# Kernel tuning notes

Measured on AMD Instinct MI355X. Metric: run time of the kernel, lower is better.

The kernel has to match this reference:

```python
import jax, jax.numpy as jnp
import numpy as np

B, L, E, V, H, M, O = 16, 64, 256, 16000, 8, 4, 2
DH = E // H
START = 0

def _pe():
    pos = np.arange(L, dtype=np.float32)[:, None]
    div = np.exp(np.arange(0, E, 2, dtype=np.float32) * (-np.log(10000.0) / E))
    pe = np.zeros((L, E), dtype=np.float32)
    pe[:, 0::2] = np.sin(pos * div)
    pe[:, 1::2] = np.cos(pos * div)
    return jnp.asarray(pe)

PE = _pe()  # [L, E] sinusoidal positional encoding (dropout p=0.0)


def setup_inputs() -> dict:
    key = jax.random.key(0)
    ks = jax.random.split(key, 16)
    g = lambda k, sh, sc: jax.random.normal(k, sh, jnp.float32) * sc
    return {
        'noise': jax.random.normal(ks[0], (B, L), jnp.float32),
        'inEmb_W': g(ks[1], (M, L, L), 1.0 / np.sqrt(L)),   # M stacked Linear(L, L), [in,out] layout
        'inEmb_b': jnp.zeros((M, L), jnp.float32),
        'Wq': g(ks[2], (O, E, E), 1.0 / np.sqrt(E)),
        'bq': jnp.zeros((O, E), jnp.float32),
        'Wk': g(ks[3], (O, E, E), 1.0 / np.sqrt(E)),
        'bk': jnp.zeros((O, E), jnp.float32),
        'Wv': g(ks[4], (O, E, E), 1.0 / np.sqrt(E)),
        'bv': jnp.zeros((O, E), jnp.float32),
        'Wo': g(ks[5], (O, E, E), 1.0 / np.sqrt(E)),
        'bo': jnp.zeros((O, E), jnp.float32),
        'ln_g': jnp.ones((O, E), jnp.float32),
        'ln_b': jnp.zeros((O, E), jnp.float32),
        'emb': g(ks[6], (V, E), 1.0),                       # Word2Vec embedding table
        'soft_W': g(ks[7], (E, V), 1.0 / np.sqrt(E)),       # soft head Linear(E, V)
        'soft_b': jnp.zeros((V,), jnp.float32),
    }


def _ln(x, g, b):
    mu = x.mean(-1, keepdims=True)
    var = ((x - mu) ** 2).mean(-1, keepdims=True)
    return (x - mu) / jnp.sqrt(var + 1e-5) * g + b


def _mha_norm(kv, q, Wq, bq, Wk, bk, Wv, bv, Wo, bo, g, b, kmask):
    # MHAwithNorm: attn(query=q, key=kv, value=kv) -> out proj -> residual -> LayerNorm
    Q = (q @ Wq + bq).reshape(B, L, H, DH)
    K = (kv @ Wk + bk).reshape(B, L, H, DH)
    Vh = (kv @ Wv + bv).reshape(B, L, H, DH)
    s = jnp.einsum('bqhd,bkhd->bhqk', Q, K) / np.sqrt(DH)
    s = jnp.where(kmask[None, None, None, :], s, -1e9)  # only the tok generated positions are valid keys
    a = jax.nn.softmax(s, axis=-1)
    o = jnp.einsum('bhqk,bkhd->bqhd', a, Vh).reshape(B, L, E)
    return _ln(o @ Wo + bo + q, g, b)


def _decode(noise, inEmb_W, inEmb_b, Wq, bq, Wk, bk, Wv, bv, Wo, bo, ln_g, ln_b, emb, soft_W, soft_b):
    w = noise
    for i in range(M):
        w = w @ inEmb_W[i] + inEmb_b[i]
    w = jnp.broadcast_to(w[:, :, None], (B, L, E))  # unsqueeze(-1).repeat(1,1,E)

    Y0 = jnp.zeros((B, L, E), jnp.float32).at[:, 0].set(emb[START] + PE[0])

    def step(Y, tok):
        kmask = jnp.arange(L) < tok  # current sequence length == tok
        out = Y
        for i in range(O):  # cross-attn blocks against w[:, :tok]
            out = _mha_norm(w, out, Wq[i], bq[i], Wk[i], bk[i], Wv[i], bv[i], Wo[i], bo[i], ln_g[i], ln_b[i], kmask)
        for i in range(O):  # same blocks reused as self-attn (faithful to source)
            out = _mha_norm(out, out, Wq[i], bq[i], Wk[i], bk[i], Wv[i], bv[i], Wo[i], bo[i], ln_g[i], ln_b[i], kmask)
        logits = out[:, tok - 1] @ soft_W + soft_b
        probs = jax.nn.softmax(logits, axis=-1)
        nxt = jnp.argmax(probs, axis=-1)  # [B]
        Y = Y.at[:, tok].set(emb[nxt] + PE[tok])
        return Y, (nxt, probs)

    _, (toks, probs) = jax.lax.scan(step, Y0, jnp.arange(1, L))
    return toks, probs  # toks [L-1, B] int, probs [L-1, B, V]


def reference(noise, inEmb_W, inEmb_b, Wq, bq, Wk, bk, Wv, bv, Wo, bo, ln_g, ln_b, emb, soft_W, soft_b):
    toks, _ = _decode(noise, inEmb_W, inEmb_b, Wq, bq, Wk, bk, Wv, bv, Wo, bo, ln_g, ln_b, emb, soft_W, soft_b)
    # torch.stack(out_sent[0]): generated token ids of batch element 0, incl. <START>
    return jnp.concatenate([jnp.array([START], dtype=toks.dtype), toks[:, 0]])
```

## Files before the change

### kernel.cpp

```cpp
#include <hip/hip_runtime.h>
#include <stdint.h>


#define NWG 128
#define NT 256

__device__ __forceinline__ float ld_c(const float* p){
  return __hip_atomic_load(p, __ATOMIC_RELAXED, __HIP_MEMORY_SCOPE_AGENT);
}
__device__ __forceinline__ void st_c(float* p, float v){
  __hip_atomic_store(p, v, __ATOMIC_RELAXED, __HIP_MEMORY_SCOPE_AGENT);
}
__device__ __forceinline__ int ld_fi(const int* p){
  return __hip_atomic_load(p, __ATOMIC_RELAXED, __HIP_MEMORY_SCOPE_AGENT);
}
__device__ __forceinline__ void st_fi(int* p, int v){
  __hip_atomic_store(p, v, __ATOMIC_RELAXED, __HIP_MEMORY_SCOPE_AGENT);
}

__device__ __forceinline__ float wredsum(float v){
#pragma unroll
  for (int m=32;m;m>>=1) v += __shfl_xor(v,m,64);
  return v;
}
__device__ __forceinline__ float wredmax(float v){
#pragma unroll
  for (int m=32;m;m>>=1) v = fmaxf(v,__shfl_xor(v,m,64));
  return v;
}
__device__ __forceinline__ float g32sum(float v){
#pragma unroll
  for (int m=16;m;m>>=1) v += __shfl_xor(v,m,64);
  return v;
}
__device__ __forceinline__ float g32max(float v){
#pragma unroll
  for (int m=16;m;m>>=1) v = fmaxf(v,__shfl_xor(v,m,64));
  return v;
}
__device__ __forceinline__ unsigned long long shflx64(unsigned long long v,int m){
  unsigned int lo=(unsigned int)(v&0xffffffffull), hi=(unsigned int)(v>>32);
  lo=__shfl_xor(lo,m,64); hi=__shfl_xor(hi,m,64);
  return (((unsigned long long)hi)<<32)|(unsigned long long)lo;
}

__device__ __forceinline__ float pe_val(int l, int e){
  int j = e >> 1;
  float dv = expf((float)(2*j) * (-0.035977892078031970f));
  float arg = (float)l * dv;
  return (e & 1) ? cosf(arg) : sinf(arg);
}

__device__ __forceinline__ void gbar_f(int* arr, int* rel, int ep){
  __syncthreads();
  if (threadIdx.x==0){
    __builtin_amdgcn_fence(__ATOMIC_RELEASE, "agent");
    __hip_atomic_store(arr + blockIdx.x*16, ep, __ATOMIC_RELAXED, __HIP_MEMORY_SCOPE_AGENT);
  }
  if (blockIdx.x==0){
    if (threadIdx.x < NWG){
      while (__hip_atomic_load(arr + threadIdx.x*16, __ATOMIC_RELAXED, __HIP_MEMORY_SCOPE_AGENT) != ep)
        __builtin_amdgcn_s_sleep(1);
    }
    __syncthreads();
    if (threadIdx.x==0)
      __hip_atomic_store(rel, ep, __ATOMIC_RELAXED, __HIP_MEMORY_SCOPE_AGENT);
  }
  if (threadIdx.x==0){
    while (__hip_atomic_load(rel, __ATOMIC_RELAXED, __HIP_MEMORY_SCOPE_AGENT) != ep)
      __builtin_amdgcn_s_sleep(1);
    __builtin_amdgcn_fence(__ATOMIC_ACQUIRE, "agent");
  }
  __syncthreads();
}

__device__ __forceinline__ void gbar_nf(int* arr, int* rel, int ep){
  __syncthreads();
  if (threadIdx.x==0)
    __hip_atomic_store(arr + blockIdx.x*16, ep, __ATOMIC_RELAXED, __HIP_MEMORY_SCOPE_AGENT);
  if (blockIdx.x==0){
    if (threadIdx.x < NWG){
      while (__hip_atomic_load(arr + threadIdx.x*16, __ATOMIC_RELAXED, __HIP_MEMORY_SCOPE_AGENT) != ep)
        __builtin_amdgcn_s_sleep(1);
    }
    __syncthreads();
    if (threadIdx.x==0)
      __hip_atomic_store(rel, ep, __ATOMIC_RELAXED, __HIP_MEMORY_SCOPE_AGENT);
  }
  if (threadIdx.x==0){
    while (__hip_atomic_load(rel, __ATOMIC_RELAXED, __HIP_MEMORY_SCOPE_AGENT) != ep)
      __builtin_amdgcn_s_sleep(1);
  }
  __syncthreads();
}

extern "C" __global__ __launch_bounds__(256, 2)
void gen18124_kernel(const float* __restrict__ noise,
                     const float* __restrict__ iw, const float* __restrict__ ib,
                     const float* __restrict__ Wq, const float* __restrict__ bq,
                     const float* __restrict__ Wk, const float* __restrict__ bk,
                     const float* __restrict__ Wv, const float* __restrict__ bv,
                     const float* __restrict__ Wo, const float* __restrict__ bo,
                     const float* __restrict__ lng, const float* __restrict__ lnb,
                     const float* __restrict__ emb, const float* __restrict__ sw,
                     const float* __restrict__ sb,
                     int* __restrict__ out, float* __restrict__ ws)
{
  const float ISQ = 0.17677669529663687f;
  __shared__ float sm[5376];
  __shared__ unsigned long long redU[4];
  extern __shared__ float swl[];

  float* WVEC = ws;
  float* SKC  = ws+64;
  float* SVC  = ws+576;
  float* KAP  = ws+1088;
  float* UT   = ws+5184;
  float* CC   = ws+9280;
  float* BETA = ws+9792;
  unsigned long long* SLOTS = (unsigned long long*)(ws+9824);
  int* Z3F = (int*)(ws+9952);
  int* ARR = (int*)(ws+10080);
  int* REL = (int*)(ws+12128);
  float* Yg  = ws+14208;
  float* R1  = ws+30592;
  float* QB  = ws+46976;
  float* KB  = ws+63360;
  float* VB  = ws+79744;
  float* R2  = ws+96128;
  float* Z2P = ws+112512;
  float* Z3P = ws+243584;

  const int g = blockIdx.x, t = threadIdx.x;
  int ep = 0;

  {
    const int base = g*125;
#pragma unroll 8
    for (int i=t; i<256*128; i+=NT){
      int e=i>>7, c=i&127;
      float val = 0.f;
      if (c<125) val = sw[e*16000 + base + c];
      swl[i]=val;
    }
  }

  {
    int c0 = 2*g;
    float a0=Wk[t*256+c0],       a1=Wk[t*256+c0+1];
    float a2=Wk[65536+t*256+c0], a3=Wk[65536+t*256+c0+1];
    float a4=Wv[t*256+c0],       a5=Wv[t*256+c0+1];
    float a6=Wv[65536+t*256+c0], a7=Wv[65536+t*256+c0+1];
    a0=wredsum(a0); a1=wredsum(a1); a2=wredsum(a2); a3=wredsum(a3);
    a4=wredsum(a4); a5=wredsum(a5); a6=wredsum(a6); a7=wredsum(a7);
    int lane=t&63, wid=t>>6;
    if (lane==0){
      sm[wid*8+0]=a0; sm[wid*8+1]=a1; sm[wid*8+2]=a2; sm[wid*8+3]=a3;
      sm[wid*8+4]=a4; sm[wid*8+5]=a5; sm[wid*8+6]=a6; sm[wid*8+7]=a7;
    }
    __syncthreads();
    if (t<8){
      float s=sm[t]+sm[8+t]+sm[16+t]+sm[24+t];
      if (t<4) SKC[(t>>1)*256 + c0 + (t&1)] = s;
      else     SVC[((t-4)>>1)*256 + c0 + ((t-4)&1)] = s;
    }
    __syncthreads();
    if (g==0){
      if (t<64) SLOTS[t]=0ull;
      if (t<8)  Z3F[t*16]=0;
      float* wl = sm+64;
      if (t<64) wl[t] = noise[t];
      __syncthreads();
      for (int i=0;i<4;i++){
        float acc=0.f;
        if (t<64){
          for (int in_=0;in_<64;in_++) acc += wl[in_]*iw[(i*64+in_)*64+t];
          acc += ib[i*64+t];
        }
        __syncthreads();
        if (t<64) wl[t]=acc;
        __syncthreads();
      }
      if (t<64) WVEC[t]=wl[t];
    }
    if (g==1){
      Yg[t] = emb[t] + pe_val(0,t);
      if (t==0) out[0]=0;
    }
  }
  gbar_f(ARR,REL,++ep);

  {
    int c0 = 2*g;
    float p00 = bv[t]    *Wo[t*256+c0],        p01 = bv[t]    *Wo[t*256+c0+1];
    float p10 = bv[256+t]*Wo[65536+t*256+c0],  p11 = bv[256+t]*Wo[65536+t*256+c0+1];
    p00=wredsum(p00); p01=wredsum(p01); p10=wredsum(p10); p11=wredsum(p11);
    int lane=t&63, wid=t>>6;
    if (lane==0){ sm[wid*4+0]=p00; sm[wid*4+1]=p01; sm[wid*4+2]=p10; sm[wid*4+3]=p11; }
    __syncthreads();
    if (t<4){
      float s=sm[t]+sm[4+t]+sm[8+t]+sm[12+t];
      int i=t>>1, cl=t&1;
      CC[i*256+c0+cl] = s + bo[i*256+c0+cl];
    }
    if (t<32){
      int i=t>>4, h=(t>>1)&7, c=c0+(t&1);
      float s=0.f;
      for (int e2=0;e2<32;e2++) s += SVC[i*256+h*32+e2]*Wo[i*65536+(h*32+e2)*256+c];
      UT[(i*8+h)*256+c]=s;
    }
    if (t>=32 && t<64){
      int u=t-32, i=u>>4, h=(u>>1)&7, e=c0+(u&1);
      float s=0.f;
      for (int c2=0;c2<32;c2++) s += Wq[i*65536+e*256+h*32+c2]*SKC[i*256+h*32+c2];
      KAP[(i*8+h)*256+e]=s;
    }
    if (g==0 && t>=64 && t<80){
      int u=t-64, i=u>>3, h=u&7;
      float s=0.f;
      for (int c2=0;c2<32;c2++) s += bq[i*256+h*32+c2]*SKC[i*256+h*32+c2];
      BETA[i*8+h]=s;
    }
  }
  gbar_f(ARR,REL,++ep);

  for (int tok=1; tok<64; tok++){
    const int n = tok-1;

    if (g < tok){
      const int q = g;
      float* xrow = sm; float* rrow = sm+256; float* m8 = sm+512; float* redv = sm+528;
      if (q==n && tok>1){
        unsigned long long s = __hip_atomic_load(&SLOTS[n], __ATOMIC_RELAXED, __HIP_MEMORY_SCOPE_AGENT);
        int v = (int)(~(unsigned int)(s & 0xffffffffull));
        if (t==0) out[q]=v;
        float yv = emb[v*256+t] + pe_val(q,t);
        xrow[t]=yv; st_c(&Yg[q*256+t], yv);
      } else {
        xrow[t]=ld_c(&Yg[q*256+t]);
      }
      __syncthreads();
      for (int blk=0; blk<2; blk++){
        const float* src = blk ? rrow : xrow;
        int h=t>>5, j=t&31;
        float part=0.f;
        for (int jj=j; jj<256; jj+=32) part += src[jj]*KAP[(blk*8+h)*256+jj];
        part = g32sum(part);
        float alpha = (part + BETA[blk*8+h]) * ISQ;
        float s1 = (j<tok)     ? alpha*WVEC[j]    : -3.4e38f;
        float s2 = (j+32<tok)  ? alpha*WVEC[j+32] : -3.4e38f;
        float mx = g32max(fmaxf(s1,s2));
        float e1 = expf(s1-mx), e2 = expf(s2-mx);
        float sn = e1*((j<tok)?WVEC[j]:0.f) + e2*((j+32<tok)?WVEC[j+32]:0.f);
        float sd = e1+e2;
        sn=g32sum(sn); sd=g32sum(sd);
        if (j==0) m8[h]=sn/sd;
        __syncthreads();
        float x_ = blk ? rrow[t] : xrow[t];
        float z = CC[blk*256+t] + x_;
#pragma unroll
        for (int h2=0;h2<8;h2++) z += m8[h2]*UT[(blk*8+h2)*256+t];
        float ssum=wredsum(z), ssq=wredsum(z*z);
        int lane=t&63, wid=t>>6;
        if (lane==0){ redv[wid]=ssum; redv[4+wid]=ssq; }
        __syncthreads();
        float ts=redv[0]+redv[1]+redv[2]+redv[3];
        float tq=redv[4]+redv[5]+redv[6]+redv[7];
        float mu=ts*(1.f/256.f);
        float var=tq*(1.f/256.f)-mu*mu;
        float rstd=1.f/sqrtf(var+1e-5f);
        float rv=(z-mu)*rstd*lng[blk*256+t]+lnb[blk*256+t];
        __syncthreads();
        rrow[t]=rv;
        __syncthreads();
      }
      st_c(&R1[q*256+t], rrow[t]);
    }
    gbar_nf(ARR,REL,++ep);

    {
      const int h=g&7, rg=g>>3;
      float* rows4 = sm;
#pragma unroll
      for (int jj=0;jj<4;jj++) rows4[jj*256+t] = ld_c(&R1[(rg+16*jj)*256+t]);
      __syncthreads();
      int c=t&31, epp=t>>5;
      const int col=h*32+c;
      float aq[4]={0,0,0,0}, ak[4]={0,0,0,0}, av[4]={0,0,0,0};
#pragma unroll 8
      for (int e=epp*32; e<epp*32+32; e++){
        float wq_=Wq[e*256+col], wk_=Wk[e*256+col], wv_=Wv[e*256+col];
#pragma unroll
        for (int jj=0;jj<4;jj++){ float r=rows4[jj*256+e]; aq[jj]+=r*wq_; ak[jj]+=r*wk_; av[jj]+=r*wv_; }
      }
#pragma unroll
      for (int jj=0;jj<4;jj++){
        aq[jj]+=__shfl_xor(aq[jj],32,64);
        ak[jj]+=__shfl_xor(ak[jj],32,64);
        av[jj]+=__shfl_xor(av[jj],32,64);
      }
      float4* redq=(float4*)(sm+1056); float4* redk=(float4*)(sm+1568); float4* redv4=(float4*)(sm+2080);
      int lane=t&63, wid=t>>6;
      if (lane<32){
        redq[wid*32+lane]=make_float4(aq[0],aq[1],aq[2],aq[3]);
        redk[wid*32+lane]=make_float4(ak[0],ak[1],ak[2],ak[3]);
        redv4[wid*32+lane]=make_float4(av[0],av[1],av[2],av[3]);
      }
      __syncthreads();
      if (t<32){
        float4 A=redq[t],B4=redq[32+t],C4=redq[64+t],D4=redq[96+t];
        float sq[4]={A.x+B4.x+C4.x+D4.x, A.y+B4.y+C4.y+D4.y, A.z+B4.z+C4.z+D4.z, A.w+B4.w+C4.w+D4.w};
        A=redk[t];B4=redk[32+t];C4=redk[64+t];D4=redk[96+t];
        float sk[4]={A.x+B4.x+C4.x+D4.x, A.y+B4.y+C4.y+D4.y, A.z+B4.z+C4.z+D4.z, A.w+B4.w+C4.w+D4.w};
        A=redv4[t];B4=redv4[32+t];C4=redv4[64+t];D4=redv4[96+t];
        float sv[4]={A.x+B4.x+C4.x+D4.x, A.y+B4.y+C4.y+D4.y, A.z+B4.z+C4.z+D4.z, A.w+B4.w+C4.w+D4.w};
        int cc=h*32+t;
        float bq_=bq[cc], bk_=bk[cc], bv_=bv[cc];
#pragma unroll
        for (int jj=0;jj<4;jj++){
          int q_=rg+16*jj;
          if (q_<tok){
            st_c(&QB[q_*256+cc], sq[jj]+bq_);
            st_c(&KB[q_*256+cc], sk[jj]+bk_);
            st_c(&VB[q_*256+cc], sv[jj]+bv_);
          }
        }
      }
    }
    gbar_nf(ARR,REL,++ep);

    {
      const int h=g&7, rg=g>>3;
      float* Ks=sm; float* Vs=sm+2112; float* qrow=sm+4224; float* arow=sm+4352; float* o2s=sm+4608;
      int k=t>>2, f0=(t&3)*8;
      if (k<tok){
#pragma unroll
        for (int i2=0;i2<8;i2++){
          Ks[k*33+f0+i2]=ld_c(&KB[k*256+h*32+f0+i2]);
          Vs[k*33+f0+i2]=ld_c(&VB[k*256+h*32+f0+i2]);
        }
      }
      if (t<128){ int jj=t>>5, c=t&31; int q_=rg+16*jj; if (q_<tok) qrow[jj*32+c]=ld_c(&QB[q_*256+h*32+c]); }
      __syncthreads();
      int w=t>>6, lane=t&63; int q_=rg+16*w; bool ok=q_<tok;
      float sc=-3.4e38f;
      if (ok && lane<tok){
        sc=0.f;
#pragma unroll
        for (int c2=0;c2<32;c2++) sc+=qrow[w*32+c2]*Ks[lane*33+c2];
        sc*=ISQ;
      }
      float mx=wredmax(sc);
      float ex=(ok&&lane<tok)? expf(sc-mx):0.f;
      float sd=wredsum(ex);
      arow[w*64+lane]= ok ? ex/sd : 0.f;
      __syncthreads();
      int j=lane&31, half=lane>>5;
      float oa=0.f;
      if (ok){ for (int k2=half;k2<tok;k2+=2) oa+=arow[w*64+k2]*Vs[k2*33+j]; }
      oa += __shfl_xor(oa,32,64);
      if (lane<32) o2s[w*32+j]=oa;
      __syncthreads();
      float acc[4]={0,0,0,0};
#pragma unroll 8
      for (int j2=0;j2<32;j2++){
        float wv_=Wo[(h*32+j2)*256+t];
#pragma unroll
        for (int jj=0;jj<4;jj++) acc[jj]+=o2s[jj*32+j2]*wv_;
      }
#pragma unroll
      for (int jj=0;jj<4;jj++){ int q2=rg+16*jj; if (q2<tok) st_c(&Z2P[(h*64+q2)*256+t], acc[jj]); }
    }
    gbar_nf(ARR,REL,++ep);

    {
      const int h=g&7, rg=g>>3;
      float* rows4=sm; float* mus=sm+1024;
#pragma unroll
      for (int jj=0;jj<4;jj++){
        int q_=rg+16*jj;
        float z = bo[t] + ld_c(&R1[q_*256+t]);
#pragma unroll
        for (int h2=0;h2<8;h2++) z += ld_c(&Z2P[(h2*64+q_)*256+t]);
        rows4[jj*256+t]=z;
      }
      __syncthreads();
      {
        int w=t>>6, lane=t&63;
        float v0=rows4[w*256+lane], v1=rows4[w*256+64+lane], v2=rows4[w*256+128+lane], v3=rows4[w*256+192+lane];
        float s=v0+v1+v2+v3, sq2=v0*v0+v1*v1+v2*v2+v3*v3;
        s=wredsum(s); sq2=wredsum(sq2);
        if (lane==0){
          float mu=s*(1.f/256.f);
          float var=sq2*(1.f/256.f)-mu*mu;
          mus[w*2]=mu; mus[w*2+1]=1.f/sqrtf(var+1e-5f);
        }
      }
      __syncthreads();
#pragma unroll
      for (int jj=0;jj<4;jj++){
        float mu=mus[jj*2], rstd=mus[jj*2+1];
        float val=(rows4[jj*256+t]-mu)*rstd*lng[t]+lnb[t];
        rows4[jj*256+t]=val;
        int q_=rg+16*jj;
        if (h==0 && q_<tok) st_c(&R2[q_*256+t], val);
      }
      __syncthreads();
      int c=t&31, epp=t>>5;
      const int col=h*32+c;
      float aq[4]={0,0,0,0}, ak[4]={0,0,0,0}, av[4]={0,0,0,0};
#pragma unroll 8
      for (int e=epp*32; e<epp*32+32; e++){
        float wq_=Wq[65536+e*256+col], wk_=Wk[65536+e*256+col], wv_=Wv[65536+e*256+col];
#pragma unroll
        for (int jj=0;jj<4;jj++){ float r=rows4[jj*256+e]; aq[jj]+=r*wq_; ak[jj]+=r*wk_; av[jj]+=r*wv_; }
      }
#pragma unroll
      for (int jj=0;jj<4;jj++){
        aq[jj]+=__shfl_xor(aq[jj],32,64);
        ak[jj]+=__shfl_xor(ak[jj],32,64);
        av[jj]+=__shfl_xor(av[jj],32,64);
      }
      float4* redq=(float4*)(sm+1056); float4* redk=(float4*)(sm+1568); float4* redv4=(float4*)(sm+2080);
      int lane=t&63, wid=t>>6;
      if (lane<32){
        redq[wid*32+lane]=make_float4(aq[0],aq[1],aq[2],aq[3]);
        redk[wid*32+lane]=make_float4(ak[0],ak[1],ak[2],ak[3]);
        redv4[wid*32+lane]=make_float4(av[0],av[1],av[2],av[3]);
      }
      __syncthreads();
      if (t<32){
        float4 A=redq[t],B4=redq[32+t],C4=redq[64+t],D4=redq[96+t];
        float sq[4]={A.x+B4.x+C4.x+D4.x, A.y+B4.y+C4.y+D4.y, A.z+B4.z+C4.z+D4.z, A.w+B4.w+C4.w+D4.w};
        A=redk[t];B4=redk[32+t];C4=redk[64+t];D4=redk[96+t];
        float sk[4]={A.x+B4.x+C4.x+D4.x, A.y+B4.y+C4.y+D4.y, A.z+B4.z+C4.z+D4.z, A.w+B4.w+C4.w+D4.w};
        A=redv4[t];B4=redv4[32+t];C4=redv4[64+t];D4=redv4[96+t];
        float sv[4]={A.x+B4.x+C4.x+D4.x, A.y+B4.y+C4.y+D4.y, A.z+B4.z+C4.z+D4.z, A.w+B4.w+C4.w+D4.w};
        int cc=h*32+t;
#pragma unroll
        for (int jj=0;jj<4;jj++){
          int q_=rg+16*jj;
          if (q_<tok){
            st_c(&KB[q_*256+cc], sk[jj]+bk[256+cc]);
            st_c(&VB[q_*256+cc], sv[jj]+bv[256+cc]);
            if (q_==n) st_c(&QB[q_*256+cc], sq[jj]+bq[256+cc]);
          }
        }
      }
    }
    gbar_nf(ARR,REL,++ep);

    {
      const int h=g&7, rg=g>>3;
      float resid = ld_c(&R2[n*256+t]);
      if (rg == (n&15)){
        float* Ks=sm; float* Vs=sm+2112; float* qn=sm+4224; float* arow=sm+4352; float* o3s=sm+4608;
        int k=t>>2, f0=(t&3)*8;
        if (k<tok){
#pragma unroll
          for (int i2=0;i2<8;i2++){
            Ks[k*33+f0+i2]=ld_c(&KB[k*256+h*32+f0+i2]);
            Vs[k*33+f0+i2]=ld_c(&VB[k*256+h*32+f0+i2]);
          }
        }
        if (t<32) qn[t]=ld_c(&QB[n*256+h*32+t]);
        __syncthreads();
        int lane=t&63, w=t>>6;
        if (w==0){
          float sc=-3.4e38f;
          if (lane<tok){
            sc=0.f;
#pragma unroll
            for (int c2=0;c2<32;c2++) sc+=qn[c2]*Ks[lane*33+c2];
            sc*=ISQ;
          }
          float mx=wredmax(sc);
          float ex=(lane<tok)? expf(sc-mx):0.f;
          float sd=wredsum(ex);
          arow[lane]=ex/sd;
        }
        __syncthreads();
        if (w==0){
          int j=lane&31, half=lane>>5;
          float oa=0.f;
          for (int k2=half;k2<tok;k2+=2) oa+=arow[k2]*Vs[k2*33+j];
          oa+=__shfl_xor(oa,32,64);
          if (lane<32) o3s[j]=oa;
        }
        __syncthreads();
        float acc=0.f;
#pragma unroll 8
        for (int j2=0;j2<32;j2++) acc+=o3s[j2]*Wo[65536+(h*32+j2)*256+t];
        st_c(&Z3P[h*256+t], acc);
        __syncthreads();
        if (t==0) st_fi(Z3F + h*16, tok);
      }
      if (t<8){ while (ld_fi(Z3F + t*16) < tok) __builtin_amdgcn_s_sleep(1); }
      __syncthreads();
      float* outn=sm; float* redv=sm+256; float* pp=sm+512;
      float z = bo[256+t] + resid;
#pragma unroll
      for (int h2=0;h2<8;h2++) z += ld_c(&Z3P[h2*256+t]);
      float s=wredsum(z), sq2=wredsum(z*z);
      int lane=t&63, wid=t>>6;
      if (lane==0){ redv[wid]=s; redv[4+wid]=sq2; }
      __syncthreads();
      float ts=redv[0]+redv[1]+redv[2]+redv[3];
      float tq=redv[4]+redv[5]+redv[6]+redv[7];
      float mu=ts*(1.f/256.f);
      float var=tq*(1.f/256.f)-mu*mu;
      float rstd=1.f/sqrtf(var+1e-5f);
      outn[t]=(z-mu)*rstd*lng[256+t]+lnb[256+t];
      __syncthreads();
      const int c = t & 127, half = t >> 7;
      float acc = 0.f;
      if (c < 125){
        const int e0 = half*128;
#pragma unroll 8
        for (int e=e0; e<e0+128; e++) acc += outn[e]*swl[e*128+c];
      }
      if (half==1 && c<125) pp[c]=acc;
      __syncthreads();
      unsigned long long key=0ull;
      if (half==0 && c<125){
        int v=g*125+c;
        float a2 = acc + pp[c] + sb[v];
        unsigned int fb=__float_as_uint(a2);
        fb = (fb&0x80000000u)? ~fb : (fb|0x80000000u);
        key=(((unsigned long long)fb)<<32) | (unsigned long long)(~(unsigned int)v);
      }
#pragma unroll
      for (int m=32;m;m>>=1){
        unsigned long long o=shflx64(key,m);
        key = (o>key)? o : key;
      }
      if (lane==0) redU[wid]=key;
      __syncthreads();
      if (t==0){
        unsigned long long kk=redU[0];
        if (redU[1]>kk) kk=redU[1];
        if (redU[2]>kk) kk=redU[2];
        if (redU[3]>kk) kk=redU[3];
        atomicMax(&SLOTS[tok], kk);
      }
    }
    gbar_nf(ARR,REL,++ep);
  }

  if (g==0 && t==0){
    unsigned long long s=__hip_atomic_load(&SLOTS[63],__ATOMIC_RELAXED,__HIP_MEMORY_SCOPE_AGENT);
    out[63]=(int)(~(unsigned int)(s&0xffffffffull));
  }
}

extern "C" void kernel_launch(void* const* d_in, const int* in_sizes, int n_in,
                              void* d_out, int out_size, void* d_ws, size_t ws_size,
                              hipStream_t stream)
{
  (void)in_sizes; (void)n_in; (void)out_size; (void)ws_size;
  hipLaunchKernelGGL(gen18124_kernel, dim3(NWG), dim3(NT), 131072, stream,
    (const float*)d_in[0],  (const float*)d_in[1],  (const float*)d_in[2],
    (const float*)d_in[3],  (const float*)d_in[4],  (const float*)d_in[5],
    (const float*)d_in[6],  (const float*)d_in[7],  (const float*)d_in[8],
    (const float*)d_in[9],  (const float*)d_in[10], (const float*)d_in[11],
    (const float*)d_in[12], (const float*)d_in[13], (const float*)d_in[14],
    (const float*)d_in[15], (int*)d_out, (float*)d_ws);
}
```

Measured before the change: 4.126 ms.

## Replace grid barriers with per-stage point-to-point readiness flags

Result: no change. 4.138 ms (+0.3%).

```diff
diff --git a/kernel.cpp b/kernel.cpp
--- a/kernel.cpp
+++ b/kernel.cpp
@@ -108,6 +108,7 @@
 {
   const float ISQ = 0.17677669529663687f;
   __shared__ float sm[5376];
+  __shared__ float qn1[32];
   __shared__ unsigned long long redU[4];
   extern __shared__ float swl[];
 
@@ -119,17 +120,23 @@
   float* CC   = ws+9280;
   float* BETA = ws+9792;
   unsigned long long* SLOTS = (unsigned long long*)(ws+9824);
-  int* Z3F = (int*)(ws+9952);
-  int* ARR = (int*)(ws+10080);
-  int* REL = (int*)(ws+12128);
-  float* Yg  = ws+14208;
-  float* R1  = ws+30592;
-  float* QB  = ws+46976;
-  float* KB  = ws+63360;
-  float* VB  = ws+79744;
-  float* R2  = ws+96128;
-  float* Z2P = ws+112512;
-  float* Z3P = ws+243584;
+  int* Z3F  = (int*)(ws+9952);
+  int* ARR  = (int*)(ws+10080);
+  int* REL  = (int*)(ws+12128);
+  int* ROWF = (int*)(ws+12144);
+  int* BF   = (int*)(ws+13168);
+  int* CF   = (int*)(ws+15216);
+  int* EF   = (int*)(ws+17264);
+  float* Yg  = ws+19456;
+  float* R1  = ws+35840;
+  float* QB  = ws+52224;
+  float* KB  = ws+68608;
+  float* VB  = ws+84992;
+  float* KB1 = ws+101376;
+  float* VB1 = ws+117760;
+  float* R2  = ws+134144;
+  float* Z2P = ws+150528;
+  float* Z3P = ws+281600;
 
   const int g = blockIdx.x, t = threadIdx.x;
   int ep = 0;
@@ -168,6 +175,8 @@
     if (g==0){
       if (t<64) SLOTS[t]=0ull;
       if (t<8)  Z3F[t*16]=0;
+      int* FLZ = (int*)(ws+12144);
+      for (int i=t;i<7168;i+=NT) FLZ[i]=0;
       float* wl = sm+64;
       if (t<64) wl[t] = noise[t];
       __syncthreads();
@@ -224,6 +233,9 @@
   }
   gbar_f(ARR,REL,++ep);
 
+  const int h  = g&7;
+  const int rg = g>>3;
+
   for (int tok=1; tok<64; tok++){
     const int n = tok-1;
 
@@ -242,11 +254,11 @@
       __syncthreads();
       for (int blk=0; blk<2; blk++){
         const float* src = blk ? rrow : xrow;
-        int h=t>>5, j=t&31;
+        int hh=t>>5, j=t&31;
         float part=0.f;
-        for (int jj=j; jj<256; jj+=32) part += src[jj]*KAP[(blk*8+h)*256+jj];
+        for (int jj=j; jj<256; jj+=32) part += src[jj]*KAP[(blk*8+hh)*256+jj];
         part = g32sum(part);
-        float alpha = (part + BETA[blk*8+h]) * ISQ;
+        float alpha = (part + BETA[blk*8+hh]) * ISQ;
         float s1 = (j<tok)     ? alpha*WVEC[j]    : -3.4e38f;
         float s2 = (j+32<tok)  ? alpha*WVEC[j+32] : -3.4e38f;
         float mx = g32max(fmaxf(s1,s2));
@@ -254,7 +266,7 @@
         float sn = e1*((j<tok)?WVEC[j]:0.f) + e2*((j+32<tok)?WVEC[j+32]:0.f);
         float sd = e1+e2;
         sn=g32sum(sn); sd=g32sum(sd);
-        if (j==0) m8[h]=sn/sd;
+        if (j==0) m8[hh]=sn/sd;
         __syncthreads();
         float x_ = blk ? rrow[t] : xrow[t];
         float z = CC[blk*256+t] + x_;
@@ -275,11 +287,16 @@
         __syncthreads();
       }
       st_c(&R1[q*256+t], rrow[t]);
-    }
-    gbar_nf(ARR,REL,++ep);
+      __syncthreads();
+      if (t==0) st_fi(ROWF + g*16, tok);
+    }
 
     {
-      const int h=g&7, rg=g>>3;
+      if (t<4){
+        int q_ = rg + 16*t;
+        if (q_ < tok){ while (ld_fi(ROWF + q_*16) < tok) __builtin_amdgcn_s_sleep(1); }
+      }
+      __syncthreads();
       float* rows4 = sm;
 #pragma unroll
       for (int jj=0;jj<4;jj++) rows4[jj*256+t] = ld_c(&R1[(rg+16*jj)*256+t]);
@@ -326,11 +343,13 @@
           }
         }
       }
-    }
-    gbar_nf(ARR,REL,++ep);
+      __syncthreads();
+      if (t==0) st_fi(BF + g*16, tok);
+    }
 
     {
-      const int h=g&7, rg=g>>3;
+      if (t<16){ while (ld_fi(BF + (t*8+h)*16) < tok) __builtin_amdgcn_s_sleep(1); }
+      __syncthreads();
       float* Ks=sm; float* Vs=sm+2112; float* qrow=sm+4224; float* arow=sm+4352; float* o2s=sm+4608;
       int k=t>>2, f0=(t&3)*8;
       if (k<tok){
@@ -370,11 +389,13 @@
       }
 #pragma unroll
       for (int jj=0;jj<4;jj++){ int q2=rg+16*jj; if (q2<tok) st_c(&Z2P[(h*64+q2)*256+t], acc[jj]); }
-    }
-    gbar_nf(ARR,REL,++ep);
+      __syncthreads();
+      if (t==0) st_fi(CF + g*16, tok);
+    }
 
     {
-      const int h=g&7, rg=g>>3;
+      if (t<8){ while (ld_fi(CF + (rg*8+t)*16) < tok) __builtin_amdgcn_s_sleep(1); }
+      __syncthreads();
       float* rows4=sm; float* mus=sm+1024;
 #pragma unroll
       for (int jj=0;jj<4;jj++){
@@ -403,7 +424,7 @@
         float val=(rows4[jj*256+t]-mu)*rstd*lng[t]+lnb[t];
         rows4[jj*256+t]=val;
         int q_=rg+16*jj;
-        if (h==0 && q_<tok) st_c(&R2[q_*256+t], val);
+        if (h==0 && q_==n) st_c(&R2[q_*256+t], val);
       }
       __syncthreads();
       int c=t&31, epp=t>>5;
@@ -441,29 +462,35 @@
         for (int jj=0;jj<4;jj++){
           int q_=rg+16*jj;
           if (q_<tok){
-            st_c(&KB[q_*256+cc], sk[jj]+bk[256+cc]);
-            st_c(&VB[q_*256+cc], sv[jj]+bv[256+cc]);
-            if (q_==n) st_c(&QB[q_*256+cc], sq[jj]+bq[256+cc]);
+            st_c(&KB1[q_*256+cc], sk[jj]+bk[256+cc]);
+            st_c(&VB1[q_*256+cc], sv[jj]+bv[256+cc]);
           }
-        }
-      }
-    }
-    gbar_nf(ARR,REL,++ep);
+          if (q_==n) qn1[t]=sq[jj]+bq[256+cc];
+        }
+      }
+      __syncthreads();
+      if (t==0) st_fi(EF + g*16, tok);
+    }
 
     {
-      const int h=g&7, rg=g>>3;
+      if (rg == (n&15)){
+        if (t<16){ while (ld_fi(EF + (t*8+h)*16) < tok) __builtin_amdgcn_s_sleep(1); }
+        if (t==16){ while (ld_fi(EF + ((n&15)*8)*16) < tok) __builtin_amdgcn_s_sleep(1); }
+      } else {
+        if (t==0){ while (ld_fi(EF + ((n&15)*8)*16) < tok) __builtin_amdgcn_s_sleep(1); }
+      }
+      __syncthreads();
       float resid = ld_c(&R2[n*256+t]);
       if (rg == (n&15)){
-        float* Ks=sm; float* Vs=sm+2112; float* qn=sm+4224; float* arow=sm+4352; float* o3s=sm+4608;
+        float* Ks=sm; float* Vs=sm+2112; float* arow=sm+4352; float* o3s=sm+4608;
         int k=t>>2, f0=(t&3)*8;
         if (k<tok){
 #pragma unroll
           for (int i2=0;i2<8;i2++){
-            Ks[k*33+f0+i2]=ld_c(&KB[k*256+h*32+f0+i2]);
-            Vs[k*33+f0+i2]=ld_c(&VB[k*256+h*32+f0+i2]);
+            Ks[k*33+f0+i2]=ld_c(&KB1[k*256+h*32+f0+i2]);
+            Vs[k*33+f0+i2]=ld_c(&VB1[k*256+h*32+f0+i2]);
           }
         }
-        if (t<32) qn[t]=ld_c(&QB[n*256+h*32+t]);
         __syncthreads();
         int lane=t&63, w=t>>6;
         if (w==0){
@@ -471,7 +498,7 @@
           if (lane<tok){
             sc=0.f;
 #pragma unroll
-            for (int c2=0;c2<32;c2++) sc+=qn[c2]*Ks[lane*33+c2];
+            for (int c2=0;c2<32;c2++) sc+=qn1[c2]*Ks[lane*33+c2];
             sc*=ISQ;
           }
           float mx=wredmax(sc);
```

## Keep per-block rows, queries and alpha in LDS instead of global scratch

Applied to the files above, without the earlier changes.

Measured after the change: 4.478 ms. 1.09x slower.

```diff
diff --git a/kernel.cpp b/kernel.cpp
--- a/kernel.cpp
+++ b/kernel.cpp
@@ -107,7 +107,12 @@
                      int* __restrict__ out, float* __restrict__ ws)
 {
   const float ISQ = 0.17677669529663687f;
-  __shared__ float sm[5376];
+  __shared__ float sm[4800];
+  __shared__ float xp[256];
+  __shared__ float r1p[1024];
+  __shared__ float qs[128];
+  __shared__ float qn1[32];
+  __shared__ float a8p[8];
   __shared__ unsigned long long redU[4];
   extern __shared__ float swl[];
 
@@ -122,14 +127,12 @@
   int* Z3F = (int*)(ws+9952);
   int* ARR = (int*)(ws+10080);
   int* REL = (int*)(ws+12128);
-  float* Yg  = ws+14208;
-  float* R1  = ws+30592;
-  float* QB  = ws+46976;
-  float* KB  = ws+63360;
-  float* VB  = ws+79744;
-  float* R2  = ws+96128;
-  float* Z2P = ws+112512;
-  float* Z3P = ws+243584;
+  float* R1  = ws+14208;
+  float* KB  = ws+30592;
+  float* VB  = ws+46976;
+  float* R2  = ws+63360;
+  float* Z2P = ws+79744;
+  float* Z3P = ws+210816;
 
   const int g = blockIdx.x, t = threadIdx.x;
   int ep = 0;
@@ -168,6 +171,7 @@
     if (g==0){
       if (t<64) SLOTS[t]=0ull;
       if (t<8)  Z3F[t*16]=0;
+      xp[t] = emb[t] + pe_val(0,t);
       float* wl = sm+64;
       if (t<64) wl[t] = noise[t];
       __syncthreads();
@@ -183,10 +187,7 @@
       }
       if (t<64) WVEC[t]=wl[t];
     }
-    if (g==1){
-      Yg[t] = emb[t] + pe_val(0,t);
-      if (t==0) out[0]=0;
-    }
+    if (g==1 && t==0) out[0]=0;
   }
   gbar_f(ARR,REL,++ep);
 
@@ -204,49 +205,59 @@
       CC[i*256+c0+cl] = s + bo[i*256+c0+cl];
     }
     if (t<32){
-      int i=t>>4, h=(t>>1)&7, c=c0+(t&1);
+      int i=t>>4, h2=(t>>1)&7, c=c0+(t&1);
       float s=0.f;
-      for (int e2=0;e2<32;e2++) s += SVC[i*256+h*32+e2]*Wo[i*65536+(h*32+e2)*256+c];
-      UT[(i*8+h)*256+c]=s;
+      for (int e2=0;e2<32;e2++) s += SVC[i*256+h2*32+e2]*Wo[i*65536+(h2*32+e2)*256+c];
+      UT[(i*8+h2)*256+c]=s;
     }
     if (t>=32 && t<64){
-      int u=t-32, i=u>>4, h=(u>>1)&7, e=c0+(u&1);
+      int u=t-32, i=u>>4, h2=(u>>1)&7, e=c0+(u&1);
       float s=0.f;
-      for (int c2=0;c2<32;c2++) s += Wq[i*65536+e*256+h*32+c2]*SKC[i*256+h*32+c2];
-      KAP[(i*8+h)*256+e]=s;
+      for (int c2=0;c2<32;c2++) s += Wq[i*65536+e*256+h2*32+c2]*SKC[i*256+h2*32+c2];
+      KAP[(i*8+h2)*256+e]=s;
     }
     if (g==0 && t>=64 && t<80){
-      int u=t-64, i=u>>3, h=u&7;
+      int u=t-64, i=u>>3, h2=u&7;
       float s=0.f;
-      for (int c2=0;c2<32;c2++) s += bq[i*256+h*32+c2]*SKC[i*256+h*32+c2];
-      BETA[i*8+h]=s;
+      for (int c2=0;c2<32;c2++) s += bq[i*256+h2*32+c2]*SKC[i*256+h2*32+c2];
+      BETA[i*8+h2]=s;
     }
   }
   gbar_f(ARR,REL,++ep);
+
+  const int h  = g&7;
+  const int rg = g>>3;
 
   for (int tok=1; tok<64; tok++){
     const int n = tok-1;
 
     if (g < tok){
       const int q = g;
-      float* xrow = sm; float* rrow = sm+256; float* m8 = sm+512; float* redv = sm+528;
+      float* rrow = sm+256; float* m8 = sm+512; float* redv = sm+528;
+      bool fresh;
       if (q==n && tok>1){
         unsigned long long s = __hip_atomic_load(&SLOTS[n], __ATOMIC_RELAXED, __HIP_MEMORY_SCOPE_AGENT);
         int v = (int)(~(unsigned int)(s & 0xffffffffull));
         if (t==0) out[q]=v;
-        float yv = emb[v*256+t] + pe_val(q,t);
-        xrow[t]=yv; st_c(&Yg[q*256+t], yv);
+        xp[t] = emb[v*256+t] + pe_val(q,t);
+        fresh = true;
       } else {
-        xrow[t]=ld_c(&Yg[q*256+t]);
+        fresh = (tok==1);
       }
       __syncthreads();
       for (int blk=0; blk<2; blk++){
-        const float* src = blk ? rrow : xrow;
-        int h=t>>5, j=t&31;
-        float part=0.f;
-        for (int jj=j; jj<256; jj+=32) part += src[jj]*KAP[(blk*8+h)*256+jj];
-        part = g32sum(part);
-        float alpha = (part + BETA[blk*8+h]) * ISQ;
+        const float* src = blk ? rrow : xp;
+        int hh=t>>5, j=t&31;
+        float alpha;
+        if (blk==1 || fresh){
+          float part=0.f;
+          for (int jj=j; jj<256; jj+=32) part += src[jj]*KAP[(blk*8+hh)*256+jj];
+          part = g32sum(part);
+          alpha = (part + BETA[blk*8+hh]) * ISQ;
+          if (blk==0 && j==0) a8p[hh]=alpha;
+        } else {
+          alpha = a8p[hh];
+        }
         float s1 = (j<tok)     ? alpha*WVEC[j]    : -3.4e38f;
         float s2 = (j+32<tok)  ? alpha*WVEC[j+32] : -3.4e38f;
         float mx = g32max(fmaxf(s1,s2));
@@ -254,9 +265,9 @@
         float sn = e1*((j<tok)?WVEC[j]:0.f) + e2*((j+32<tok)?WVEC[j+32]:0.f);
         float sd = e1+e2;
         sn=g32sum(sn); sd=g32sum(sd);
-        if (j==0) m8[h]=sn/sd;
-        __syncthreads();
-        float x_ = blk ? rrow[t] : xrow[t];
+        if (j==0) m8[hh]=sn/sd;
+        __syncthreads();
+        float x_ = blk ? rrow[t] : xp[t];
         float z = CC[blk*256+t] + x_;
 #pragma unroll
         for (int h2=0;h2<8;h2++) z += m8[h2]*UT[(blk*8+h2)*256+t];
@@ -279,10 +290,8 @@
     gbar_nf(ARR,REL,++ep);
 
     {
-      const int h=g&7, rg=g>>3;
-      float* rows4 = sm;
-#pragma unroll
-      for (int jj=0;jj<4;jj++) rows4[jj*256+t] = ld_c(&R1[(rg+16*jj)*256+t]);
+#pragma unroll
+      for (int jj=0;jj<4;jj++) r1p[jj*256+t] = ld_c(&R1[(rg+16*jj)*256+t]);
       __syncthreads();
       int c=t&31, epp=t>>5;
       const int col=h*32+c;
@@ -291,7 +300,7 @@
       for (int e=epp*32; e<epp*32+32; e++){
         float wq_=Wq[e*256+col], wk_=Wk[e*256+col], wv_=Wv[e*256+col];
 #pragma unroll
-        for (int jj=0;jj<4;jj++){ float r=rows4[jj*256+e]; aq[jj]+=r*wq_; ak[jj]+=r*wk_; av[jj]+=r*wv_; }
+        for (int jj=0;jj<4;jj++){ float r=r1p[jj*256+e]; aq[jj]+=r*wq_; ak[jj]+=r*wk_; av[jj]+=r*wv_; }
       }
 #pragma unroll
       for (int jj=0;jj<4;jj++){
@@ -318,9 +327,9 @@
         float bq_=bq[cc], bk_=bk[cc], bv_=bv[cc];
 #pragma unroll
         for (int jj=0;jj<4;jj++){
+          qs[jj*32+t]=sq[jj]+bq_;
           int q_=rg+16*jj;
           if (q_<tok){
-            st_c(&QB[q_*256+cc], sq[jj]+bq_);
             st_c(&KB[q_*256+cc], sk[jj]+bk_);
             st_c(&VB[q_*256+cc], sv[jj]+bv_);
           }
@@ -330,8 +339,7 @@
     gbar_nf(ARR,REL,++ep);
 
     {
-      const int h=g&7, rg=g>>3;
-      float* Ks=sm; float* Vs=sm+2112; float* qrow=sm+4224; float* arow=sm+4352; float* o2s=sm+4608;
+      float* Ks=sm; float* Vs=sm+2112; float* arow=sm+4352; float* o2s=sm+4608;
       int k=t>>2, f0=(t&3)*8;
       if (k<tok){
 #pragma unroll
@@ -340,14 +348,13 @@
           Vs[k*33+f0+i2]=ld_c(&VB[k*256+h*32+f0+i2]);
         }
       }
-      if (t<128){ int jj=t>>5, c=t&31; int q_=rg+16*jj; if (q_<tok) qrow[jj*32+c]=ld_c(&QB[q_*256+h*32+c]); }
       __syncthreads();
       int w=t>>6, lane=t&63; int q_=rg+16*w; bool ok=q_<tok;
       float sc=-3.4e38f;
       if (ok && lane<tok){
         sc=0.f;
 #pragma unroll
-        for (int c2=0;c2<32;c2++) sc+=qrow[w*32+c2]*Ks[lane*33+c2];
+        for (int c2=0;c2<32;c2++) sc+=qs[w*32+c2]*Ks[lane*33+c2];
         sc*=ISQ;
       }
       float mx=wredmax(sc);
@@ -374,12 +381,11 @@
     gbar_nf(ARR,REL,++ep);
 
     {
-      const int h=g&7, rg=g>>3;
       float* rows4=sm; float* mus=sm+1024;
 #pragma unroll
       for (int jj=0;jj<4;jj++){
         int q_=rg+16*jj;
-        float z = bo[t] + ld_c(&R1[q_*256+t]);
+        float z = bo[t] + r1p[jj*256+t];
 #pragma unroll
         for (int h2=0;h2<8;h2++) z += ld_c(&Z2P[(h2*64+q_)*256+t]);
         rows4[jj*256+t]=z;
@@ -403,7 +409,7 @@
         float val=(rows4[jj*256+t]-mu)*rstd*lng[t]+lnb[t];
         rows4[jj*256+t]=val;
         int q_=rg+16*jj;
-        if (h==0 && q_<tok) st_c(&R2[q_*256+t], val);
+        if (h==0 && q_==n) st_c(&R2[q_*256+t], val);
       }
       __syncthreads();
       int c=t&31, epp=t>>5;
@@ -443,18 +449,17 @@
           if (q_<tok){
             st_c(&KB[q_*256+cc], sk[jj]+bk[256+cc]);
             st_c(&VB[q_*256+cc], sv[jj]+bv[256+cc]);
-            if (q_==n) st_c(&QB[q_*256+cc], sq[jj]+bq[256+cc]);
           }
+          if (q_==n) qn1[t]=sq[jj]+bq[256+cc];
         }
       }
     }
     gbar_nf(ARR,REL,++ep);
 
     {
-      const int h=g&7, rg=g>>3;
       float resid = ld_c(&R2[n*256+t]);
       if (rg == (n&15)){
-        float* Ks=sm; float* Vs=sm+2112; float* qn=sm+4224; float* arow=sm+4352; float* o3s=sm+4608;
+        float* Ks=sm; float* Vs=sm+2112; float* arow=sm+4352; float* o3s=sm+4608;
         int k=t>>2, f0=(t&3)*8;
         if (k<tok){
 #pragma unroll
@@ -463,7 +468,6 @@
             Vs[k*33+f0+i2]=ld_c(&VB[k*256+h*32+f0+i2]);
           }
         }
-        if (t<32) qn[t]=ld_c(&QB[n*256+h*32+t]);
         __syncthreads();
         int lane=t&63, w=t>>6;
         if (w==0){
@@ -471,7 +475,7 @@
           if (lane<tok){
             sc=0.f;
 #pragma unroll
-            for (int c2=0;c2<32;c2++) sc+=qn[c2]*Ks[lane*33+c2];
+            for (int c2=0;c2<32;c2++) sc+=qn1[c2]*Ks[lane*33+c2];
             sc*=ISQ;
           }
           float mx=wredmax(sc);
```

## Remove per-token grid barrier by precomputing next-step cross-attn rows in idle blocks

Applied to the files above, without the earlier changes.

After: 4.042 ms. 2.0% less time.

```diff
diff --git a/kernel.cpp b/kernel.cpp
--- a/kernel.cpp
+++ b/kernel.cpp
@@ -49,6 +49,48 @@
   float dv = expf((float)(2*j) * (-0.035977892078031970f));
   float arg = (float)l * dv;
   return (e & 1) ? cosf(arg) : sinf(arg);
+}
+
+__device__ __forceinline__ void a_chain(const float* xrow, float* rrow,
+    float* m8, float* redv,
+    const float* KAP, const float* BETA, const float* WVEC,
+    const float* CC, const float* UT,
+    const float* lng, const float* lnb, int tokm, int t){
+  const float ISQ = 0.17677669529663687f;
+  for (int blk=0; blk<2; blk++){
+    const float* src = blk ? rrow : xrow;
+    int hh=t>>5, j=t&31;
+    float part=0.f;
+    for (int jj=j; jj<256; jj+=32) part += src[jj]*KAP[(blk*8+hh)*256+jj];
+    part = g32sum(part);
+    float alpha = (part + BETA[blk*8+hh]) * ISQ;
+    float s1 = (j<tokm)     ? alpha*WVEC[j]    : -3.4e38f;
+    float s2 = (j+32<tokm)  ? alpha*WVEC[j+32] : -3.4e38f;
+    float mx = g32max(fmaxf(s1,s2));
+    float e1 = expf(s1-mx), e2 = expf(s2-mx);
+    float sn = e1*((j<tokm)?WVEC[j]:0.f) + e2*((j+32<tokm)?WVEC[j+32]:0.f);
+    float sd = e1+e2;
+    sn=g32sum(sn); sd=g32sum(sd);
+    if (j==0) m8[hh]=sn/sd;
+    __syncthreads();
+    float x_ = blk ? rrow[t] : xrow[t];
+    float z = CC[blk*256+t] + x_;
+#pragma unroll
+    for (int h2=0;h2<8;h2++) z += m8[h2]*UT[(blk*8+h2)*256+t];
+    float ssum=wredsum(z), ssq=wredsum(z*z);
+    int lane=t&63, wid=t>>6;
+    if (lane==0){ redv[wid]=ssum; redv[4+wid]=ssq; }
+    __syncthreads();
+    float ts=redv[0]+redv[1]+redv[2]+redv[3];
+    float tq=redv[4]+redv[5]+redv[6]+redv[7];
+    float mu=ts*(1.f/256.f);
+    float var=tq*(1.f/256.f)-mu*mu;
+    float rstd=1.f/sqrtf(var+1e-5f);
+    float rv=(z-mu)*rstd*lng[blk*256+t]+lnb[blk*256+t];
+    __syncthreads();
+    rrow[t]=rv;
+    __syncthreads();
+  }
 }
 
 __device__ __forceinline__ void gbar_f(int* arr, int* rel, int ep){
@@ -204,85 +246,57 @@
       CC[i*256+c0+cl] = s + bo[i*256+c0+cl];
     }
     if (t<32){
-      int i=t>>4, h=(t>>1)&7, c=c0+(t&1);
+      int i=t>>4, h2=(t>>1)&7, c=c0+(t&1);
       float s=0.f;
-      for (int e2=0;e2<32;e2++) s += SVC[i*256+h*32+e2]*Wo[i*65536+(h*32+e2)*256+c];
-      UT[(i*8+h)*256+c]=s;
+      for (int e2=0;e2<32;e2++) s += SVC[i*256+h2*32+e2]*Wo[i*65536+(h2*32+e2)*256+c];
+      UT[(i*8+h2)*256+c]=s;
     }
     if (t>=32 && t<64){
-      int u=t-32, i=u>>4, h=(u>>1)&7, e=c0+(u&1);
+      int u=t-32, i=u>>4, h2=(u>>1)&7, e=c0+(u&1);
       float s=0.f;
-      for (int c2=0;c2<32;c2++) s += Wq[i*65536+e*256+h*32+c2]*SKC[i*256+h*32+c2];
-      KAP[(i*8+h)*256+e]=s;
+      for (int c2=0;c2<32;c2++) s += Wq[i*65536+e*256+h2*32+c2]*SKC[i*256+h2*32+c2];
+      KAP[(i*8+h2)*256+e]=s;
     }
     if (g==0 && t>=64 && t<80){
-      int u=t-64, i=u>>3, h=u&7;
+      int u=t-64, i=u>>3, h2=u&7;
       float s=0.f;
-      for (int c2=0;c2<32;c2++) s += bq[i*256+h*32+c2]*SKC[i*256+h*32+c2];
-      BETA[i*8+h]=s;
+      for (int c2=0;c2<32;c2++) s += bq[i*256+h2*32+c2]*SKC[i*256+h2*32+c2];
+      BETA[i*8+h2]=s;
     }
   }
   gbar_f(ARR,REL,++ep);
+
+  if (g==0){
+    float* axr=sm; float* arr=sm+256; float* am8=sm+512; float* ard=sm+528;
+    axr[t]=ld_c(&Yg[t]);
+    __syncthreads();
+    a_chain(axr,arr,am8,ard, KAP,BETA,WVEC,CC,UT,lng,lnb, 1, t);
+    st_c(&R1[t], arr[t]);
+  }
+  gbar_f(ARR,REL,++ep);
+
+  const int h  = g&7;
+  const int rg = g>>3;
 
   for (int tok=1; tok<64; tok++){
     const int n = tok-1;
 
-    if (g < tok){
-      const int q = g;
-      float* xrow = sm; float* rrow = sm+256; float* m8 = sm+512; float* redv = sm+528;
-      if (q==n && tok>1){
+    {
+      float* rows4 = sm;
+#pragma unroll
+      for (int jj=0;jj<4;jj++) rows4[jj*256+t] = ld_c(&R1[(rg+16*jj)*256+t]);
+      if (tok>1 && rg==(n&15)){
+        float* axr=sm+2700; float* arr2=sm+2956; float* am8=sm+3212; float* ard=sm+3224;
         unsigned long long s = __hip_atomic_load(&SLOTS[n], __ATOMIC_RELAXED, __HIP_MEMORY_SCOPE_AGENT);
         int v = (int)(~(unsigned int)(s & 0xffffffffull));
-        if (t==0) out[q]=v;
-        float yv = emb[v*256+t] + pe_val(q,t);
-        xrow[t]=yv; st_c(&Yg[q*256+t], yv);
-      } else {
-        xrow[t]=ld_c(&Yg[q*256+t]);
-      }
-      __syncthreads();
-      for (int blk=0; blk<2; blk++){
-        const float* src = blk ? rrow : xrow;
-        int h=t>>5, j=t&31;
-        float part=0.f;
-        for (int jj=j; jj<256; jj+=32) part += src[jj]*KAP[(blk*8+h)*256+jj];
-        part = g32sum(part);
-        float alpha = (part + BETA[blk*8+h]) * ISQ;
-        float s1 = (j<tok)     ? alpha*WVEC[j]    : -3.4e38f;
-        float s2 = (j+32<tok)  ? alpha*WVEC[j+32] : -3.4e38f;
-        float mx = g32max(fmaxf(s1,s2));
-        float e1 = expf(s1-mx), e2 = expf(s2-mx);
-        float sn = e1*((j<tok)?WVEC[j]:0.f) + e2*((j+32<tok)?WVEC[j+32]:0.f);
-        float sd = e1+e2;
-        sn=g32sum(sn); sd=g32sum(sd);
-        if (j==0) m8[h]=sn/sd;
-        __syncthreads();
-        float x_ = blk ? rrow[t] : xrow[t];
-        float z = CC[blk*256+t] + x_;
-#pragma unroll
-        for (int h2=0;h2<8;h2++) z += m8[h2]*UT[(blk*8+h2)*256+t];
-        float ssum=wredsum(z), ssq=wredsum(z*z);
-        int lane=t&63, wid=t>>6;
-        if (lane==0){ redv[wid]=ssum; redv[4+wid]=ssq; }
-        __syncthreads();
-        float ts=redv[0]+redv[1]+redv[2]+redv[3];
-        float tq=redv[4]+redv[5]+redv[6]+redv[7];
-        float mu=ts*(1.f/256.f);
-        float var=tq*(1.f/256.f)-mu*mu;
-        float rstd=1.f/sqrtf(var+1e-5f);
-        float rv=(z-mu)*rstd*lng[blk*256+t]+lnb[blk*256+t];
-        __syncthreads();
-        rrow[t]=rv;
-        __syncthreads();
-      }
-      st_c(&R1[q*256+t], rrow[t]);
-    }
-    gbar_nf(ARR,REL,++ep);
-
-    {
-      const int h=g&7, rg=g>>3;
-      float* rows4 = sm;
-#pragma unroll
-      for (int jj=0;jj<4;jj++) rows4[jj*256+t] = ld_c(&R1[(rg+16*jj)*256+t]);
+        if (h==0 && t==0) out[n]=v;
+        axr[t] = emb[v*256+t] + pe_val(n,t);
+        if (h==0) st_c(&Yg[n*256+t], axr[t]);
+        __syncthreads();
+        a_chain(axr,arr2,am8,ard, KAP,BETA,WVEC,CC,UT,lng,lnb, tok, t);
+        rows4[(n>>4)*256+t] = arr2[t];
+        if (h==0) st_c(&R1[n*256+t], arr2[t]);
+      }
       __syncthreads();
       int c=t&31, epp=t>>5;
       const int col=h*32+c;
@@ -330,7 +344,6 @@
     gbar_nf(ARR,REL,++ep);
 
     {
-      const int h=g&7, rg=g>>3;
       float* Ks=sm; float* Vs=sm+2112; float* qrow=sm+4224; float* arow=sm+4352; float* o2s=sm+4608;
       int k=t>>2, f0=(t&3)*8;
       if (k<tok){
@@ -374,7 +387,6 @@
     gbar_nf(ARR,REL,++ep);
 
     {
-      const int h=g&7, rg=g>>3;
       float* rows4=sm; float* mus=sm+1024;
 #pragma unroll
       for (int jj=0;jj<4;jj++){
@@ -403,7 +415,7 @@
         float val=(rows4[jj*256+t]-mu)*rstd*lng[t]+lnb[t];
         rows4[jj*256+t]=val;
         int q_=rg+16*jj;
-        if (h==0 && q_<tok) st_c(&R2[q_*256+t], val);
+        if (h==0 && q_==n) st_c(&R2[q_*256+t], val);
       }
       __syncthreads();
       int c=t&31, epp=t>>5;
@@ -451,19 +463,19 @@
     gbar_nf(ARR,REL,++ep);
 
     {
-      const int h=g&7, rg=g>>3;
       float resid = ld_c(&R2[n*256+t]);
-      if (rg == (n&15)){
+      if (g < 8){
+        const int hh = g;
         float* Ks=sm; float* Vs=sm+2112; float* qn=sm+4224; float* arow=sm+4352; float* o3s=sm+4608;
         int k=t>>2, f0=(t&3)*8;
         if (k<tok){
 #pragma unroll
           for (int i2=0;i2<8;i2++){
-            Ks[k*33+f0+i2]=ld_c(&KB[k*256+h*32+f0+i2]);
-            Vs[k*33+f0+i2]=ld_c(&VB[k*256+h*32+f0+i2]);
+            Ks[k*33+f0+i2]=ld_c(&KB[k*256+hh*32+f0+i2]);
+            Vs[k*33+f0+i2]=ld_c(&VB[k*256+hh*32+f0+i2]);
           }
         }
-        if (t<32) qn[t]=ld_c(&QB[n*256+h*32+t]);
+        if (t<32) qn[t]=ld_c(&QB[n*256+hh*32+t]);
         __syncthreads();
         int lane=t&63, w=t>>6;
         if (w==0){
@@ -490,10 +502,19 @@
         __syncthreads();
         float acc=0.f;
 #pragma unroll 8
-        for (int j2=0;j2<32;j2++) acc+=o3s[j2]*Wo[65536+(h*32+j2)*256+t];
-        st_c(&Z3P[h*256+t], acc);
-        __syncthreads();
-        if (t==0) st_fi(Z3F + h*16, tok);
+        for (int j2=0;j2<32;j2++) acc+=o3s[j2]*Wo[65536+(hh*32+j2)*256+t];
+        st_c(&Z3P[hh*256+t], acc);
+        __syncthreads();
+        if (t==0) st_fi(Z3F + hh*16, tok);
+      } else if (g>=64 && g<127){
+        const int q = g-64;
+        if (q < tok && tok < 63){
+          float* axr=sm; float* arr2=sm+256; float* am8=sm+512; float* ard=sm+528;
+          axr[t]=ld_c(&Yg[q*256+t]);
+          __syncthreads();
+          a_chain(axr,arr2,am8,ard, KAP,BETA,WVEC,CC,UT,lng,lnb, tok+1, t);
+          st_c(&R1[q*256+t], arr2[t]);
+        }
       }
       if (t<8){ while (ld_fi(Z3F + t*16) < tok) __builtin_amdgcn_s_sleep(1); }
       __syncthreads();
```
